# Kernel optimization log

Hardware: AMD Instinct MI355X
Metric: run time of the kernel (lower is better)

## Reference

```python
import jax, jax.numpy as jnp
import numpy as np

B, N, D, OUT, NUM_ITERS = 8, 4096, 1024, 1024, 3
LN_EPS = 1e-5


def setup_inputs() -> dict:
    key = jax.random.key(0)
    ks = jax.random.split(key, 8)
    s = (6.0 / (2 * D)) ** 0.5  # xavier-uniform-like scale
    return {
        "query": jax.random.normal(ks[0], (B, D), jnp.float32),
        "feat": jax.random.normal(ks[1], (B, N, D), jnp.float32),
        "W_h": jax.random.uniform(ks[2], (D, D), jnp.float32, -s, s),
        "W_f": jax.random.uniform(ks[3], (D, D), jnp.float32, -s, s),
        "W_g": jax.random.normal(ks[4], (4, D, D), jnp.float32) / np.sqrt(D),
        "ln_w": jnp.ones((D,), jnp.float32),
        "ln_b": jnp.zeros((D,), jnp.float32),
        "W_out": jax.random.uniform(ks[5], (OUT, D), jnp.float32, -s, s),
        "b_out": jnp.zeros((OUT,), jnp.float32),
        "feat_mask": jax.random.bernoulli(ks[6], 0.2, (B, 1, 1, N)),
    }


def _layer_norm(x, w, b):
    mu = x.mean(-1, keepdims=True)
    var = jnp.var(x, axis=-1, keepdims=True)
    return (x - mu) / jnp.sqrt(var + LN_EPS) * w + b


def reference(query, feat, W_h, W_f, W_g, ln_w, ln_b, W_out, b_out, feat_mask):
    q = query @ W_h                       # [B, D]
    f = feat @ W_f                        # [B, N, D]
    mask = feat_mask.reshape(feat.shape[0], feat.shape[1])  # squeeze(1).squeeze(1)
    b = jnp.where(mask, jnp.float32(-1e18), jnp.float32(0.0))  # [B, N]
    # feat_group is iteration-invariant: mean over the 4 orthogonal transforms
    # mean_g(f @ W_g[g].T) == f @ mean_g(W_g).T
    fg = f @ W_g.mean(0).T                # [B, N, D]
    n = fg.shape[1]
    for i in range(NUM_ITERS):
        c = jax.nn.softmax(b, axis=1)     # [B, N]
        if i == NUM_ITERS - 1:
            out = jnp.einsum('bn,bnd->bd', c, fg)
        else:
            delta = jnp.einsum('bd,bnd->bn', q, fg)
            delta = (delta - delta.mean(1, keepdims=True)) / (
                delta.std(1, keepdims=True, ddof=1) + 1e-9)  # torch.std is unbiased
            b = b + delta
            out = jnp.einsum('bn,bnd->bd', c, fg) / n  # mean over dim 1
        q = _layer_norm(q + jax.nn.selu(out), ln_w, ln_b)
    return q @ W_out.T + b_out
```

## Files before the change

kernel.cpp:

```cpp
#include <hip/hip_runtime.h>
#include <hip/hip_bf16.h>


using u16 = unsigned short;
using u32 = unsigned int;
using u8  = unsigned char;
using u64 = unsigned long long;

#define SELU_L 1.0507009873554805f
#define SELU_A 1.6732632423543772f

__device__ float g_M[1048576];
__device__ float g_q[8192];
__device__ float g_qc[8192];
__device__ float g_t[8192];
__device__ float g_u[8192];
__device__ float g_s[8192];
__device__ float g_bst[32768];
__device__ float g_c[32768];
__device__ float g_delta[32768];
__device__ float g_outv[8192];
__device__ float g_outv2[8192];
__device__ float g_v[8192];
__device__ int   g_dt[12];

__device__ __forceinline__ float blo(u32 u){ return __uint_as_float(u << 16); }
__device__ __forceinline__ float bhi(u32 u){ return __uint_as_float(u & 0xffff0000u); }
__device__ __forceinline__ float b2f(u16 u){ return __uint_as_float(((u32)u) << 16); }

__device__ __forceinline__ void unpack8(uint4 x, float* f){
  f[0]=blo(x.x); f[1]=bhi(x.x); f[2]=blo(x.y); f[3]=bhi(x.y);
  f[4]=blo(x.z); f[5]=bhi(x.z); f[6]=blo(x.w); f[7]=bhi(x.w);
}

__device__ __forceinline__ float ldf(const void* p, size_t i, int dt){
  return dt ? ((const float*)p)[i] : b2f(((const u16*)p)[i]);
}
__device__ __forceinline__ void load8(const void* base, size_t idx, int dt, float* f){
  if (dt == 0) {
    uint4 x = *(const uint4*)((const u16*)base + idx);
    unpack8(x, f);
  } else {
    const float* p = (const float*)base + idx;
    float4 a = *(const float4*)p, b = *(const float4*)(p + 4);
    f[0]=a.x; f[1]=a.y; f[2]=a.z; f[3]=a.w; f[4]=b.x; f[5]=b.y; f[6]=b.z; f[7]=b.w;
  }
}

__device__ __forceinline__ float wredsum(float x){
#pragma unroll
  for (int o = 32; o; o >>= 1) x += __shfl_xor(x, o, 64);
  return x;
}

__device__ __forceinline__ bool mon(const u8* maskp, int e, int mode){
  if (mode == 0) return maskp[e] != 0;
  if (mode == 1) return ((const int*)maskp)[e] != 0;
  if (mode == 2 || mode == 4) return ((const u16*)maskp)[e] != 0;
  if (mode == 3) return ((const u32*)maskp)[e] != 0;
  return ((const u64*)maskp)[e] != 0ULL;
}

__global__ void kdet(const void* p0, const void* p1, const void* p2, const void* p3,
                     const void* p4, const void* p5, const void* p6, const void* p7,
                     const void* p8, const void* p9)
{
  const void* ps[10] = {p0,p1,p2,p3,p4,p5,p6,p7,p8,p9};
  int tid = threadIdx.x;
  int w = tid >> 6, lane = tid & 63;
  if (w < 9) {
    const u16* wp = (const u16*)ps[w];
    u16 x0 = wp[lane], x1 = wp[64 + lane];
    int e0 = (x0 >> 7) & 0xFF, e1 = (x1 >> 7) & 0xFF;
    u64 nz0 = __ballot(x0 != 0), nz1 = __ballot(x1 != 0);
    u64 pa0 = __ballot(x0 != 0 && e0 >= 0x70 && e0 <= 0x8F);
    u64 pa1 = __ballot(x1 != 0 && e1 >= 0x70 && e1 <= 0x8F);
    if (lane == 0) {
      const u64 evenm = 0x5555555555555555ULL;
      int nz = __popcll(nz0) + __popcll(nz1);
      int pass = __popcll(pa0) + __popcll(pa1);
      int evenNZ = __popcll(nz0 & evenm) + __popcll(nz1 & evenm);
      int oddNZ  = nz - evenNZ;
      int dt;
      if (nz == 0)                    dt = 0;
      else if (evenNZ == 0 && oddNZ)  dt = 1;
      else                            dt = (pass * 10 >= nz * 9) ? 0 : 1;
      g_dt[w] = dt;
    }
  } else if (w == 9) {
    const u8* mp = (const u8*)ps[9];
    u64 v = ((const u64*)mp)[lane];
    bool f16c=false, isF=false, nz01=false, nzNon4=false, nzM8_4=false, anynz=false;
#pragma unroll
    for (int j = 0; j < 8; ++j) {
      u8 cb = (u8)(v >> (8 * j));
      if (!cb) continue;
      int i = lane * 8 + j;
      anynz = true;
      if (cb == 0x3C && (i & 1)) f16c = true;
      if (cb == 0x3F || cb == 0x80) isF = true;
      int m = i & 3;
      if (m == 0 || m == 1) nz01 = true;
      if (m != 0) nzNon4 = true;
      if ((i & 7) == 4) nzM8_4 = true;
    }
    bool A  = __ballot(f16c)   != 0;
    bool Bf = __ballot(isF)    != 0;
    bool C  = __ballot(nz01)   != 0;
    bool Dn = __ballot(nzNon4) != 0;
    bool E  = __ballot(nzM8_4) != 0;
    bool F  = __ballot(anynz)  != 0;
    if (lane == 0) {
      int mode;
      if (A)       mode = 4;
      else if (Bf) mode = C ? 2 : 3;
      else if (Dn) mode = 0;
      else if (E)  mode = 1;
      else if (F)  mode = 5;
      else         mode = 1;
      g_dt[9] = mode;
    }
  }
  for (int i = tid; i < 8192; i += 640) {
    g_q[i] = 0.f; g_t[i] = 0.f; g_u[i] = 0.f; g_s[i] = 0.f;
  }
}

__global__ void __launch_bounds__(256)
kprep(const void* __restrict__ Wg, const void* __restrict__ Wh,
      const void* __restrict__ query, const u8* __restrict__ maskp)
{
  int blk = blockIdx.x, tid = threadIdx.x;
  if (blk < 1024) {
    int dtg = g_dt[4];
    int e = blk * 1024 + tid * 4;
    float a0=0.f,a1=0.f,a2=0.f,a3=0.f;
#pragma unroll
    for (int g = 0; g < 4; ++g) {
      size_t o = (size_t)g * 1048576 + e;
      a0 += ldf(Wg, o+0, dtg); a1 += ldf(Wg, o+1, dtg);
      a2 += ldf(Wg, o+2, dtg); a3 += ldf(Wg, o+3, dtg);
    }
    *(float4*)(g_M + e) = make_float4(a0*0.25f, a1*0.25f, a2*0.25f, a3*0.25f);
  } else if (blk < 1088) {
    int dtq = g_dt[0], dth = g_dt[2];
    __shared__ float ql[512];
    int blk2 = blk - 1024;
    int kt = blk2 & 3, dc = blk2 >> 2;
    for (int idx = tid; idx < 512; idx += 256) {
      int b = idx >> 6, d = idx & 63;
      ql[idx] = ldf(query, b * 1024 + dc * 64 + d, dtq);
    }
    __syncthreads();
    int k = kt * 256 + tid;
    float acc[8] = {0,0,0,0,0,0,0,0};
    for (int dd = 0; dd < 64; ++dd) {
      int d = dc * 64 + dd;
      float w = ldf(Wh, (size_t)d * 1024 + k, dth);
#pragma unroll
      for (int b = 0; b < 8; ++b) acc[b] += ql[(b << 6) + dd] * w;
    }
#pragma unroll
    for (int b = 0; b < 8; ++b) atomicAdd(&g_q[b * 1024 + k], acc[b]);
  } else if (blk < 1120) {
    int mode = g_dt[9];
    int e0 = (blk - 1088) * 1024 + tid * 4;
#pragma unroll
    for (int j = 0; j < 4; ++j) {
      int e = e0 + j;
      g_bst[e] = mon(maskp, e, mode) ? -1e18f : 0.f;
    }
  } else {
    __shared__ int sc[256];
    int mode = g_dt[9];
    int b = blk - 1120;
    u32 bits = 0; int cnt = 0;
#pragma unroll
    for (int r = 0; r < 16; ++r) {
      int n = tid + 256 * r;
      bool on = mon(maskp, b * 4096 + n, mode);
      if (on) bits |= (1u << r); else ++cnt;
    }
    sc[tid] = cnt; __syncthreads();
    for (int s2 = 128; s2; s2 >>= 1) { if (tid < s2) sc[tid] += sc[tid + s2]; __syncthreads(); }
    int ct = sc[0];
    float inv = 1.f / (float)(ct ? ct : 4096);
    float moff = ct ? 0.f : inv;
#pragma unroll
    for (int r = 0; r < 16; ++r) {
      int n = tid + 256 * r;
      g_c[b * 4096 + n] = ((bits >> r) & 1u) ? moff : inv;
    }
  }
}

__device__ __forceinline__ void build_ql(float* ql, const float* qsrc,
                                         const float* osrc, float scale,
                                         const void* lnw, const void* lnb, int tid)
{
  int w = tid >> 6, lane = tid & 63;
  int dtw = g_dt[5], dtb = g_dt[6];
#pragma unroll
  for (int rr = 0; rr < 2; ++rr) {
    int b = w + rr * 4;
    const float* qb = qsrc + b * 1024;
    const float* ob = osrc + b * 1024;
    float x[16]; float sum = 0.f, sq = 0.f;
#pragma unroll
    for (int cc = 0; cc < 4; ++cc) {
      float4 qv = *(const float4*)(qb + cc * 256 + lane * 4);
      float4 ov = *(const float4*)(ob + cc * 256 + lane * 4);
      float q4[4] = {qv.x, qv.y, qv.z, qv.w};
      float o4[4] = {ov.x, ov.y, ov.z, ov.w};
#pragma unroll
      for (int e = 0; e < 4; ++e) {
        float o = o4[e] * scale;
        float se = (o > 0.f) ? SELU_L * o : SELU_L * SELU_A * expm1f(o);
        float val = q4[e] + se;
        x[cc * 4 + e] = val; sum += val; sq += val * val;
      }
    }
    sum = wredsum(sum); sq = wredsum(sq);
    float mean = sum * (1.f / 1024.f);
    float var = fmaxf(sq * (1.f / 1024.f) - mean * mean, 0.f);
    float rstd = rsqrtf(var + 1e-5f);
#pragma unroll
    for (int cc = 0; cc < 4; ++cc)
#pragma unroll
      for (int e = 0; e < 4; ++e) {
        int d = cc * 256 + lane * 4 + e;
        ql[b * 1024 + d] = (x[cc * 4 + e] - mean) * rstd * ldf(lnw, d, dtw)
                           + ldf(lnb, d, dtb);
      }
  }
  __syncthreads();
}

__global__ void __launch_bounds__(256)
kt(const void* __restrict__ lnw, const void* __restrict__ lnb, int phase)
{
  __shared__ float ql[8192];
  int blk = blockIdx.x, tid = threadIdx.x;
  if (blk >= 256) {
    int b = blk - 256;
    *(float4*)(g_u + b * 1024 + tid * 4) = make_float4(0.f, 0.f, 0.f, 0.f);
    return;
  }
  if (phase == 0) {
    for (int i = tid; i < 8192; i += 256) ql[i] = g_q[i];
    __syncthreads();
  } else {
    build_ql(ql, g_qc, g_outv, 1.f / 4096.f, lnw, lnb, tid);
  }
  if (blk == 0) {
    for (int i = tid; i < 8192; i += 256) g_qc[i] = ql[i];
  }
  int jt = blk & 3, dc4 = blk >> 2;
  int j = jt * 256 + tid;
  float acc[8] = {0,0,0,0,0,0,0,0};
  for (int dd = 0; dd < 16; ++dd) {
    int d = dc4 * 16 + dd;
    float mv = g_M[(size_t)d * 1024 + j];
#pragma unroll
    for (int b = 0; b < 8; ++b) acc[b] += ql[(b << 10) + d] * mv;
  }
#pragma unroll
  for (int b = 0; b < 8; ++b) atomicAdd(&g_t[b * 1024 + j], acc[b]);
}

__global__ void __launch_bounds__(256) kv(const void* __restrict__ Wf)
{
  __shared__ float shm[8192];
  int tid = threadIdx.x;
  int dtf = g_dt[3];
  for (int i = tid; i < 8192; i += 256) shm[i] = g_t[i];
  __syncthreads();
  int w = tid >> 6, lane = tid & 63;
  int k = blockIdx.x * 4 + w;
  size_t row = (size_t)k * 1024;
  float f[16];
  load8(Wf, row + lane * 8, dtf, f);
  load8(Wf, row + 512 + lane * 8, dtf, f + 8);
  float acc[8];
#pragma unroll
  for (int b = 0; b < 8; ++b) {
    const float* tb = shm + b * 1024;
    float d = 0.f;
#pragma unroll
    for (int j = 0; j < 8; ++j) d += f[j]     * tb[lane * 8 + j];
#pragma unroll
    for (int j = 0; j < 8; ++j) d += f[8 + j] * tb[512 + lane * 8 + j];
    acc[b] = wredsum(d);
  }
  if (lane == 0) {
#pragma unroll
    for (int b = 0; b < 8; ++b) g_v[b * 1024 + k] = acc[b];
  }
}

__global__ void __launch_bounds__(256)
kfd(const void* __restrict__ feat, int need_delta)
{
  __shared__ float sl[4][1024];
  int blkx = blockIdx.x, tid = threadIdx.x;
  if (blkx >= 512) {
    int b = blkx - 512;
    *(float4*)(g_u + b * 1024 + tid * 4) = make_float4(0.f, 0.f, 0.f, 0.f);
    return;
  }
  int w = tid >> 6, lane = tid & 63;
  int b = blkx >> 6, ch = blkx & 63;
  int dtf = g_dt[1];
  float vr[16];
#pragma unroll
  for (int j = 0; j < 16; ++j) vr[j] = 0.f;
  if (need_delta) {
    const float* vb = g_v + b * 1024;
#pragma unroll
    for (int j = 0; j < 8; ++j) { vr[j] = vb[lane * 8 + j]; vr[8 + j] = vb[512 + lane * 8 + j]; }
  }
  float acc[16];
#pragma unroll
  for (int j = 0; j < 16; ++j) acc[j] = 0.f;
  int n0 = ch * 64 + w * 16;
  for (int r = 0; r < 16; ++r) {
    int n = n0 + r;
    size_t row = ((size_t)b * 4096 + n) * 1024;
    float f[16];
    load8(feat, row + lane * 8, dtf, f);
    load8(feat, row + 512 + lane * 8, dtf, f + 8);
    float cn = g_c[b * 4096 + n];
#pragma unroll
    for (int j = 0; j < 16; ++j) acc[j] += cn * f[j];
    if (need_delta) {
      float dot = 0.f;
#pragma unroll
      for (int j = 0; j < 16; ++j) dot += f[j] * vr[j];
      dot = wredsum(dot);
      if (lane == 0) g_delta[b * 4096 + n] = dot;
    }
  }
#pragma unroll
  for (int j = 0; j < 8; ++j) {
    sl[w][lane * 8 + j] = acc[j];
    sl[w][512 + lane * 8 + j] = acc[8 + j];
  }
  __syncthreads();
#pragma unroll
  for (int j = 0; j < 4; ++j) {
    int k = tid * 4 + j;
    float val = sl[0][k] + sl[1][k] + sl[2][k] + sl[3][k];
    atomicAdd(&g_s[b * 1024 + k], val);
  }
}

__global__ void __launch_bounds__(256)
ksu(const void* __restrict__ Wf, int do_stats)
{
  __shared__ float sm[256];
  int blk = blockIdx.x, tid = threadIdx.x;
  if (blk < 8) {
    if (!do_stats) return;
    int b = blk;
    const float* row = g_delta + b * 4096;
    float xs[16], sum = 0.f, sq = 0.f;
#pragma unroll
    for (int r = 0; r < 16; ++r) { float x = row[tid + 256 * r]; xs[r] = x; sum += x; sq += x * x; }
    sm[tid] = sum; __syncthreads();
    for (int s2 = 128; s2; s2 >>= 1) { if (tid < s2) sm[tid] += sm[tid + s2]; __syncthreads(); }
    sum = sm[0]; __syncthreads();
    sm[tid] = sq; __syncthreads();
    for (int s2 = 128; s2; s2 >>= 1) { if (tid < s2) sm[tid] += sm[tid + s2]; __syncthreads(); }
    sq = sm[0];
    float mean = sum / 4096.f;
    float var = fmaxf((sq - 4096.f * mean * mean) / 4095.f, 0.f);
    float inv = 1.f / (sqrtf(var) + 1e-9f);
#pragma unroll
    for (int r = 0; r < 16; ++r) {
      int i = tid + 256 * r;
      g_bst[b * 4096 + i] += (xs[r] - mean) * inv;
    }
    return;
  }
  int dtf = g_dt[3];
  int blk2 = blk - 8;
  int jt = blk2 & 3, kc4 = blk2 >> 2;
  if (tid < 128) {
    int b = tid >> 4, kk = tid & 15;
    sm[tid] = g_s[b * 1024 + kc4 * 16 + kk];
  }
  __syncthreads();
  int j = jt * 256 + tid;
  float acc[8] = {0,0,0,0,0,0,0,0};
  for (int kk = 0; kk < 16; ++kk) {
    int k = kc4 * 16 + kk;
    float w = ldf(Wf, (size_t)k * 1024 + j, dtf);
#pragma unroll
    for (int b = 0; b < 8; ++b) acc[b] += sm[(b << 4) + kk] * w;
  }
#pragma unroll
  for (int b = 0; b < 8; ++b) atomicAdd(&g_u[b * 1024 + j], acc[b]);
}

__global__ void __launch_bounds__(256) kout(int dst2)
{
  __shared__ float sh[8192];
  int blk = blockIdx.x, tid = threadIdx.x;
  if (blk >= 256) {
    if (blk < 264) {
      int b = blk - 256;
      const float* row = g_bst + b * 4096;
      float mx = -3.4e38f;
      for (int i = tid; i < 4096; i += 256) mx = fmaxf(mx, row[i]);
      sh[tid] = mx; __syncthreads();
      for (int s2 = 128; s2; s2 >>= 1) { if (tid < s2) sh[tid] = fmaxf(sh[tid], sh[tid + s2]); __syncthreads(); }
      mx = sh[0]; __syncthreads();
      float sum = 0.f;
      for (int i = tid; i < 4096; i += 256) {
        float e = __expf(row[i] - mx);
        g_c[b * 4096 + i] = e; sum += e;
      }
      sh[tid] = sum; __syncthreads();
      for (int s2 = 128; s2; s2 >>= 1) { if (tid < s2) sh[tid] += sh[tid + s2]; __syncthreads(); }
      float inv = 1.f / sh[0];
      for (int i = tid; i < 4096; i += 256) g_c[b * 4096 + i] *= inv;
    } else if (blk < 272) {
      int b = blk - 264;
      *(float4*)(g_t + b * 1024 + tid * 4) = make_float4(0.f, 0.f, 0.f, 0.f);
    } else {
      int b = blk - 272;
      *(float4*)(g_s + b * 1024 + tid * 4) = make_float4(0.f, 0.f, 0.f, 0.f);
    }
    return;
  }
  float* dst = dst2 ? g_outv2 : g_outv;
  for (int i = tid; i < 8192; i += 256) sh[i] = g_u[i];
  __syncthreads();
  int w = tid >> 6, lane = tid & 63;
  int d = blk * 4 + w;
  const float* row = g_M + (size_t)d * 1024;
  float f[16];
#pragma unroll
  for (int cc = 0; cc < 4; ++cc) {
    float4 x = *(const float4*)(row + cc * 256 + lane * 4);
    f[cc*4+0]=x.x; f[cc*4+1]=x.y; f[cc*4+2]=x.z; f[cc*4+3]=x.w;
  }
  float acc[8];
#pragma unroll
  for (int b = 0; b < 8; ++b) {
    const float* ub = sh + b * 1024;
    float dd = 0.f;
#pragma unroll
    for (int cc = 0; cc < 4; ++cc)
#pragma unroll
      for (int e = 0; e < 4; ++e) dd += f[cc * 4 + e] * ub[cc * 256 + lane * 4 + e];
    acc[b] = wredsum(dd);
  }
  if (lane == 0) {
#pragma unroll
    for (int b = 0; b < 8; ++b) dst[b * 1024 + d] = acc[b];
  }
}

__global__ void __launch_bounds__(256)
kfin(const void* __restrict__ Wout, const void* __restrict__ bout,
     const void* __restrict__ lnw, const void* __restrict__ lnb,
     float* __restrict__ out)
{
  __shared__ float ql[8192];
  int tid = threadIdx.x;
  build_ql(ql, g_qc, g_outv, 1.f / 4096.f, lnw, lnb, tid);
  build_ql(ql, ql, g_outv2, 1.f, lnw, lnb, tid);
  int w = tid >> 6, lane = tid & 63;
  int o = blockIdx.x * 4 + w;
  int dto = g_dt[7], dtb = g_dt[8];
  size_t row = (size_t)o * 1024;
  float f[16];
  load8(Wout, row + lane * 8, dto, f);
  load8(Wout, row + 512 + lane * 8, dto, f + 8);
  float acc[8];
#pragma unroll
  for (int b = 0; b < 8; ++b) {
    const float* qb = ql + b * 1024;
    float d = 0.f;
#pragma unroll
    for (int j = 0; j < 8; ++j) d += f[j]     * qb[lane * 8 + j];
#pragma unroll
    for (int j = 0; j < 8; ++j) d += f[8 + j] * qb[512 + lane * 8 + j];
    acc[b] = wredsum(d);
  }
  if (lane == 0) {
    float bo = ldf(bout, o, dtb);
#pragma unroll
    for (int b = 0; b < 8; ++b) out[b * 1024 + o] = acc[b] + bo;
  }
}

extern "C" void kernel_launch(void* const* d_in, const int* in_sizes, int n_in,
                              void* d_out, int out_size, void* d_ws, size_t ws_size,
                              hipStream_t stream)
{
  const void* query = d_in[0];
  const void* feat  = d_in[1];
  const void* Wh    = d_in[2];
  const void* Wf    = d_in[3];
  const void* Wg    = d_in[4];
  const void* lnw   = d_in[5];
  const void* lnb   = d_in[6];
  const void* Wout  = d_in[7];
  const void* bout  = d_in[8];
  const u8*   maskp = (const u8*)d_in[9];
  (void)in_sizes; (void)n_in; (void)out_size; (void)d_ws; (void)ws_size;

  kdet<<<1, 640, 0, stream>>>(query, feat, Wh, Wf, Wg, lnw, lnb, Wout, bout, maskp);
  kprep<<<1128, 256, 0, stream>>>(Wg, Wh, query, maskp);

  kt<<<264, 256, 0, stream>>>(lnw, lnb, 0);
  kv<<<256, 256, 0, stream>>>(Wf);
  kfd<<<512, 256, 0, stream>>>(feat, 1);
  ksu<<<264, 256, 0, stream>>>(Wf, 1);
  kout<<<280, 256, 0, stream>>>(0);
  kt<<<264, 256, 0, stream>>>(lnw, lnb, 1);
  kv<<<256, 256, 0, stream>>>(Wf);
  kfd<<<512, 256, 0, stream>>>(feat, 1);
  ksu<<<264, 256, 0, stream>>>(Wf, 1);
  kout<<<280, 256, 0, stream>>>(0);
  kfd<<<520, 256, 0, stream>>>(feat, 0);
  ksu<<<264, 256, 0, stream>>>(Wf, 0);
  kout<<<256, 256, 0, stream>>>(1);
  kfin<<<256, 256, 0, stream>>>(Wout, bout, lnw, lnb, (float*)d_out);
}
```

Before: 421.8 us.

## Vectorize loads, double kfd grid, fuse softmax into ksu stats, stage Wh in LDS

The feat-streaming kernel kfd now launches 1024 blocks with 8 rows per wave instead of 512 blocks with 16, to expose more parallelism. Its per-row softmax weights are loaded once as float4. The softmax over b is moved from kout into the ksu statistics blocks, fusing the b update with max/exp/normalize and saving a global round trip. kprep handles 8 Wg elements per thread and stages Wh tiles through shared memory for coalesced reads. Many global and shared copies are widened to float4 with explicit alignment. The changes add more synchronisation in the stats blocks and make the atomics in kfd finer grained.

Measured after the change: 426.1 us. No clear change (+1.0%).

```diff
diff --git a/kernel.cpp b/kernel.cpp
--- a/kernel.cpp
+++ b/kernel.cpp
@@ -10,19 +10,19 @@
 #define SELU_L 1.0507009873554805f
 #define SELU_A 1.6732632423543772f
 
-__device__ float g_M[1048576];
-__device__ float g_q[8192];
-__device__ float g_qc[8192];
-__device__ float g_t[8192];
-__device__ float g_u[8192];
-__device__ float g_s[8192];
-__device__ float g_bst[32768];
-__device__ float g_c[32768];
-__device__ float g_delta[32768];
-__device__ float g_outv[8192];
-__device__ float g_outv2[8192];
-__device__ float g_v[8192];
-__device__ int   g_dt[12];
+__device__ __align__(16) float g_M[1048576];
+__device__ __align__(16) float g_q[8192];
+__device__ __align__(16) float g_qc[8192];
+__device__ __align__(16) float g_t[8192];
+__device__ __align__(16) float g_u[8192];
+__device__ __align__(16) float g_s[8192];
+__device__ __align__(16) float g_bst[32768];
+__device__ __align__(16) float g_c[32768];
+__device__ __align__(16) float g_delta[32768];
+__device__ __align__(16) float g_outv[8192];
+__device__ __align__(16) float g_outv2[8192];
+__device__ __align__(16) float g_v[8192];
+__device__ int g_dt[12];
 
 __device__ __forceinline__ float blo(u32 u){ return __uint_as_float(u << 16); }
 __device__ __forceinline__ float bhi(u32 u){ return __uint_as_float(u & 0xffff0000u); }
@@ -121,8 +121,10 @@
       g_dt[9] = mode;
     }
   }
-  for (int i = tid; i < 8192; i += 640) {
-    g_q[i] = 0.f; g_t[i] = 0.f; g_u[i] = 0.f; g_s[i] = 0.f;
+  float4 z = make_float4(0.f, 0.f, 0.f, 0.f);
+  for (int i = tid; i < 2048; i += 640) {
+    ((float4*)g_q)[i] = z; ((float4*)g_t)[i] = z;
+    ((float4*)g_u)[i] = z; ((float4*)g_s)[i] = z;
   }
 }
 
@@ -130,41 +132,57 @@
 kprep(const void* __restrict__ Wg, const void* __restrict__ Wh,
       const void* __restrict__ query, const u8* __restrict__ maskp)
 {
+  __shared__ float wl[8192];
+  __shared__ float ql[512];
   int blk = blockIdx.x, tid = threadIdx.x;
-  if (blk < 1024) {
+  if (blk < 512) {
     int dtg = g_dt[4];
-    int e = blk * 1024 + tid * 4;
-    float a0=0.f,a1=0.f,a2=0.f,a3=0.f;
+    int e = blk * 2048 + tid * 8;
+    float a[8] = {0,0,0,0,0,0,0,0};
 #pragma unroll
     for (int g = 0; g < 4; ++g) {
-      size_t o = (size_t)g * 1048576 + e;
-      a0 += ldf(Wg, o+0, dtg); a1 += ldf(Wg, o+1, dtg);
-      a2 += ldf(Wg, o+2, dtg); a3 += ldf(Wg, o+3, dtg);
-    }
-    *(float4*)(g_M + e) = make_float4(a0*0.25f, a1*0.25f, a2*0.25f, a3*0.25f);
-  } else if (blk < 1088) {
+      float f[8];
+      load8(Wg, (size_t)g * 1048576 + e, dtg, f);
+#pragma unroll
+      for (int u = 0; u < 8; ++u) a[u] += f[u];
+    }
+    *(float4*)(g_M + e)     = make_float4(a[0]*0.25f, a[1]*0.25f, a[2]*0.25f, a[3]*0.25f);
+    *(float4*)(g_M + e + 4) = make_float4(a[4]*0.25f, a[5]*0.25f, a[6]*0.25f, a[7]*0.25f);
+  } else if (blk < 576) {
     int dtq = g_dt[0], dth = g_dt[2];
-    __shared__ float ql[512];
-    int blk2 = blk - 1024;
-    int kt = blk2 & 3, dc = blk2 >> 2;
+    int blk2 = blk - 512;
+    int kt4 = blk2 & 3, dc = blk2 >> 2;
     for (int idx = tid; idx < 512; idx += 256) {
-      int b = idx >> 6, d = idx & 63;
-      ql[idx] = ldf(query, b * 1024 + dc * 64 + d, dtq);
-    }
-    __syncthreads();
-    int k = kt * 256 + tid;
+      int b = idx >> 6, dl = idx & 63;
+      ql[idx] = ldf(query, b * 1024 + dc * 64 + dl, dtq);
+    }
     float acc[8] = {0,0,0,0,0,0,0,0};
-    for (int dd = 0; dd < 64; ++dd) {
-      int d = dc * 64 + dd;
-      float w = ldf(Wh, (size_t)d * 1024 + k, dth);
-#pragma unroll
-      for (int b = 0; b < 8; ++b) acc[b] += ql[(b << 6) + dd] * w;
-    }
+    int cq = tid & 31, r4 = tid >> 5;
+#pragma unroll
+    for (int h = 0; h < 2; ++h) {
+      if (h) __syncthreads();
+#pragma unroll
+      for (int u4 = 0; u4 < 4; ++u4) {
+        int r = r4 * 4 + u4;
+        float f[8];
+        load8(Wh, (size_t)(dc * 64 + h * 32 + r) * 1024 + kt4 * 256 + cq * 8, dth, f);
+#pragma unroll
+        for (int u = 0; u < 8; ++u) wl[r * 256 + cq * 8 + u] = f[u];
+      }
+      __syncthreads();
+      for (int dd = 0; dd < 32; ++dd) {
+        float w = wl[dd * 256 + tid];
+        int dl = h * 32 + dd;
+#pragma unroll
+        for (int b = 0; b < 8; ++b) acc[b] += ql[(b << 6) + dl] * w;
+      }
+    }
+    int k = kt4 * 256 + tid;
 #pragma unroll
     for (int b = 0; b < 8; ++b) atomicAdd(&g_q[b * 1024 + k], acc[b]);
-  } else if (blk < 1120) {
+  } else if (blk < 608) {
     int mode = g_dt[9];
-    int e0 = (blk - 1088) * 1024 + tid * 4;
+    int e0 = (blk - 576) * 1024 + tid * 4;
 #pragma unroll
     for (int j = 0; j < 4; ++j) {
       int e = e0 + j;
@@ -173,7 +191,7 @@
   } else {
     __shared__ int sc[256];
     int mode = g_dt[9];
-    int b = blk - 1120;
+    int b = blk - 608;
     u32 bits = 0; int cnt = 0;
 #pragma unroll
     for (int r = 0; r < 16; ++r) {
@@ -239,7 +257,7 @@
 __global__ void __launch_bounds__(256)
 kt(const void* __restrict__ lnw, const void* __restrict__ lnb, int phase)
 {
-  __shared__ float ql[8192];
+  __shared__ __align__(16) float ql[8192];
   int blk = blockIdx.x, tid = threadIdx.x;
   if (blk >= 256) {
     int b = blk - 256;
@@ -247,13 +265,15 @@
     return;
   }
   if (phase == 0) {
-    for (int i = tid; i < 8192; i += 256) ql[i] = g_q[i];
+    for (int it = tid; it < 2048; it += 256)
+      ((float4*)ql)[it] = ((const float4*)g_q)[it];
     __syncthreads();
   } else {
     build_ql(ql, g_qc, g_outv, 1.f / 4096.f, lnw, lnb, tid);
   }
   if (blk == 0) {
-    for (int i = tid; i < 8192; i += 256) g_qc[i] = ql[i];
+    for (int it = tid; it < 2048; it += 256)
+      ((float4*)g_qc)[it] = ((const float4*)ql)[it];
   }
   int jt = blk & 3, dc4 = blk >> 2;
   int j = jt * 256 + tid;
@@ -270,10 +290,11 @@
 
 __global__ void __launch_bounds__(256) kv(const void* __restrict__ Wf)
 {
-  __shared__ float shm[8192];
+  __shared__ __align__(16) float shm[8192];
   int tid = threadIdx.x;
   int dtf = g_dt[3];
-  for (int i = tid; i < 8192; i += 256) shm[i] = g_t[i];
+  for (int it = tid; it < 2048; it += 256)
+    ((float4*)shm)[it] = ((const float4*)g_t)[it];
   __syncthreads();
   int w = tid >> 6, lane = tid & 63;
   int k = blockIdx.x * 4 + w;
@@ -303,33 +324,42 @@
 {
   __shared__ float sl[4][1024];
   int blkx = blockIdx.x, tid = threadIdx.x;
-  if (blkx >= 512) {
-    int b = blkx - 512;
+  if (blkx >= 1024) {
+    int b = blkx - 1024;
     *(float4*)(g_u + b * 1024 + tid * 4) = make_float4(0.f, 0.f, 0.f, 0.f);
     return;
   }
   int w = tid >> 6, lane = tid & 63;
-  int b = blkx >> 6, ch = blkx & 63;
+  int b = blkx >> 7, ch = blkx & 127;
   int dtf = g_dt[1];
   float vr[16];
 #pragma unroll
   for (int j = 0; j < 16; ++j) vr[j] = 0.f;
   if (need_delta) {
     const float* vb = g_v + b * 1024;
-#pragma unroll
-    for (int j = 0; j < 8; ++j) { vr[j] = vb[lane * 8 + j]; vr[8 + j] = vb[512 + lane * 8 + j]; }
-  }
+    float4 v0 = *(const float4*)(vb + lane * 8);
+    float4 v1 = *(const float4*)(vb + lane * 8 + 4);
+    float4 v2 = *(const float4*)(vb + 512 + lane * 8);
+    float4 v3 = *(const float4*)(vb + 512 + lane * 8 + 4);
+    vr[0]=v0.x; vr[1]=v0.y; vr[2]=v0.z; vr[3]=v0.w;
+    vr[4]=v1.x; vr[5]=v1.y; vr[6]=v1.z; vr[7]=v1.w;
+    vr[8]=v2.x; vr[9]=v2.y; vr[10]=v2.z; vr[11]=v2.w;
+    vr[12]=v3.x; vr[13]=v3.y; vr[14]=v3.z; vr[15]=v3.w;
+  }
+  int n0 = ch * 32 + w * 8;
+  float4 c0 = *(const float4*)(g_c + b * 4096 + n0);
+  float4 c1 = *(const float4*)(g_c + b * 4096 + n0 + 4);
+  float cc[8] = {c0.x, c0.y, c0.z, c0.w, c1.x, c1.y, c1.z, c1.w};
   float acc[16];
 #pragma unroll
   for (int j = 0; j < 16; ++j) acc[j] = 0.f;
-  int n0 = ch * 64 + w * 16;
-  for (int r = 0; r < 16; ++r) {
+  for (int r = 0; r < 8; ++r) {
     int n = n0 + r;
     size_t row = ((size_t)b * 4096 + n) * 1024;
     float f[16];
     load8(feat, row + lane * 8, dtf, f);
     load8(feat, row + 512 + lane * 8, dtf, f + 8);
-    float cn = g_c[b * 4096 + n];
+    float cn = cc[r];
 #pragma unroll
     for (int j = 0; j < 16; ++j) acc[j] += cn * f[j];
     if (need_delta) {
@@ -362,24 +392,54 @@
   if (blk < 8) {
     if (!do_stats) return;
     int b = blk;
-    const float* row = g_delta + b * 4096;
-    float xs[16], sum = 0.f, sq = 0.f;
-#pragma unroll
-    for (int r = 0; r < 16; ++r) { float x = row[tid + 256 * r]; xs[r] = x; sum += x; sq += x * x; }
+    const float* drow = g_delta + b * 4096;
+    float xs[16];
+    float sum = 0.f, sq = 0.f;
+#pragma unroll
+    for (int rr = 0; rr < 4; ++rr) {
+      float4 x4 = *(const float4*)(drow + tid * 4 + rr * 1024);
+      float xx[4] = {x4.x, x4.y, x4.z, x4.w};
+#pragma unroll
+      for (int j = 0; j < 4; ++j) { xs[rr*4+j] = xx[j]; sum += xx[j]; sq += xx[j]*xx[j]; }
+    }
     sm[tid] = sum; __syncthreads();
     for (int s2 = 128; s2; s2 >>= 1) { if (tid < s2) sm[tid] += sm[tid + s2]; __syncthreads(); }
     sum = sm[0]; __syncthreads();
     sm[tid] = sq; __syncthreads();
     for (int s2 = 128; s2; s2 >>= 1) { if (tid < s2) sm[tid] += sm[tid + s2]; __syncthreads(); }
-    sq = sm[0];
+    sq = sm[0]; __syncthreads();
     float mean = sum / 4096.f;
     float var = fmaxf((sq - 4096.f * mean * mean) / 4095.f, 0.f);
     float inv = 1.f / (sqrtf(var) + 1e-9f);
-#pragma unroll
-    for (int r = 0; r < 16; ++r) {
-      int i = tid + 256 * r;
-      g_bst[b * 4096 + i] += (xs[r] - mean) * inv;
-    }
+    float* brow = g_bst + b * 4096;
+    float mx = -3.4e38f;
+#pragma unroll
+    for (int rr = 0; rr < 4; ++rr) {
+      float4 b4 = *(const float4*)(brow + tid * 4 + rr * 1024);
+      float bb[4] = {b4.x, b4.y, b4.z, b4.w};
+#pragma unroll
+      for (int j = 0; j < 4; ++j) {
+        float nb = bb[j] + (xs[rr*4+j] - mean) * inv;
+        xs[rr*4+j] = nb;
+        mx = fmaxf(mx, nb);
+      }
+      *(float4*)(brow + tid * 4 + rr * 1024) =
+          make_float4(xs[rr*4], xs[rr*4+1], xs[rr*4+2], xs[rr*4+3]);
+    }
+    sm[tid] = mx; __syncthreads();
+    for (int s2 = 128; s2; s2 >>= 1) { if (tid < s2) sm[tid] = fmaxf(sm[tid], sm[tid + s2]); __syncthreads(); }
+    mx = sm[0]; __syncthreads();
+    float es = 0.f;
+#pragma unroll
+    for (int k16 = 0; k16 < 16; ++k16) { float e = __expf(xs[k16] - mx); xs[k16] = e; es += e; }
+    sm[tid] = es; __syncthreads();
+    for (int s2 = 128; s2; s2 >>= 1) { if (tid < s2) sm[tid] += sm[tid + s2]; __syncthreads(); }
+    float cinv = 1.f / sm[0];
+    float* crow = g_c + b * 4096;
+#pragma unroll
+    for (int rr = 0; rr < 4; ++rr)
+      *(float4*)(crow + tid * 4 + rr * 1024) =
+          make_float4(xs[rr*4]*cinv, xs[rr*4+1]*cinv, xs[rr*4+2]*cinv, xs[rr*4+3]*cinv);
     return;
   }
   int dtf = g_dt[3];
@@ -404,37 +464,21 @@
 
 __global__ void __launch_bounds__(256) kout(int dst2)
 {
-  __shared__ float sh[8192];
+  __shared__ __align__(16) float sh[8192];
   int blk = blockIdx.x, tid = threadIdx.x;
   if (blk >= 256) {
     if (blk < 264) {
       int b = blk - 256;
-      const float* row = g_bst + b * 4096;
-      float mx = -3.4e38f;
-      for (int i = tid; i < 4096; i += 256) mx = fmaxf(mx, row[i]);
-      sh[tid] = mx; __syncthreads();
-      for (int s2 = 128; s2; s2 >>= 1) { if (tid < s2) sh[tid] = fmaxf(sh[tid], sh[tid + s2]); __syncthreads(); }
-      mx = sh[0]; __syncthreads();
-      float sum = 0.f;
-      for (int i = tid; i < 4096; i += 256) {
-        float e = __expf(row[i] - mx);
-        g_c[b * 4096 + i] = e; sum += e;
-      }
-      sh[tid] = sum; __syncthreads();
-      for (int s2 = 128; s2; s2 >>= 1) { if (tid < s2) sh[tid] += sh[tid + s2]; __syncthreads(); }
-      float inv = 1.f / sh[0];
-      for (int i = tid; i < 4096; i += 256) g_c[b * 4096 + i] *= inv;
-    } else if (blk < 272) {
-      int b = blk - 264;
       *(float4*)(g_t + b * 1024 + tid * 4) = make_float4(0.f, 0.f, 0.f, 0.f);
     } else {
-      int b = blk - 272;
+      int b = blk - 264;
       *(float4*)(g_s + b * 1024 + tid * 4) = make_float4(0.f, 0.f, 0.f, 0.f);
     }
     return;
   }
   float* dst = dst2 ? g_outv2 : g_outv;
-  for (int i = tid; i < 8192; i += 256) sh[i] = g_u[i];
+  for (int it = tid; it < 2048; it += 256)
+    ((float4*)sh)[it] = ((const float4*)g_u)[it];
   __syncthreads();
   int w = tid >> 6, lane = tid & 63;
   int d = blk * 4 + w;
@@ -467,7 +511,7 @@
      const void* __restrict__ lnw, const void* __restrict__ lnb,
      float* __restrict__ out)
 {
-  __shared__ float ql[8192];
+  __shared__ __align__(16) float ql[8192];
   int tid = threadIdx.x;
   build_ql(ql, g_qc, g_outv, 1.f / 4096.f, lnw, lnb, tid);
   build_ql(ql, ql, g_outv2, 1.f, lnw, lnb, tid);
@@ -513,19 +557,19 @@
   (void)in_sizes; (void)n_in; (void)out_size; (void)d_ws; (void)ws_size;
 
   kdet<<<1, 640, 0, stream>>>(query, feat, Wh, Wf, Wg, lnw, lnb, Wout, bout, maskp);
-  kprep<<<1128, 256, 0, stream>>>(Wg, Wh, query, maskp);
+  kprep<<<616, 256, 0, stream>>>(Wg, Wh, query, maskp);
 
   kt<<<264, 256, 0, stream>>>(lnw, lnb, 0);
   kv<<<256, 256, 0, stream>>>(Wf);
-  kfd<<<512, 256, 0, stream>>>(feat, 1);
+  kfd<<<1024, 256, 0, stream>>>(feat, 1);
   ksu<<<264, 256, 0, stream>>>(Wf, 1);
-  kout<<<280, 256, 0, stream>>>(0);
+  kout<<<272, 256, 0, stream>>>(0);
   kt<<<264, 256, 0, stream>>>(lnw, lnb, 1);
   kv<<<256, 256, 0, stream>>>(Wf);
-  kfd<<<512, 256, 0, stream>>>(feat, 1);
+  kfd<<<1024, 256, 0, stream>>>(feat, 1);
   ksu<<<264, 256, 0, stream>>>(Wf, 1);
-  kout<<<280, 256, 0, stream>>>(0);
-  kfd<<<520, 256, 0, stream>>>(feat, 0);
+  kout<<<272, 256, 0, stream>>>(0);
+  kfd<<<1032, 256, 0, stream>>>(feat, 0);
   ksu<<<264, 256, 0, stream>>>(Wf, 0);
   kout<<<256, 256, 0, stream>>>(1);
   kfin<<<256, 256, 0, stream>>>(Wout, bout, lnw, lnb, (float*)d_out);
```
